# Kernel tuning notes

Hardware: AMD Instinct MI355X
Metric: run time of the kernel (lower is better)

Reference implementation:

```python
import jax, jax.numpy as jnp
import numpy as np

B = 524288
H = 20          # heads
NUM_EX = 13     # embedding rows
EMB = 3         # embedding dim
FEAT_IN, FEAT_OUT = 3, 5
HEAD_IN, HEAD_HID = 8, 10


def setup_inputs() -> dict:
    key = jax.random.key(0)
    ks = jax.random.split(key, 12)
    e = jax.random.randint(ks[0], (B, H), 0, NUM_EX)
    f = jax.random.normal(ks[1], (B, H * FEAT_IN), dtype=jnp.float32)
    # embedding table; row 0 zeroed as in the torch __init__
    emb = jax.random.normal(ks[2], (NUM_EX, EMB), dtype=jnp.float32) * 0.1
    emb = emb.at[0].set(0.0)
    # features Linear(3 -> 5), stored as (in, out) so y = x @ Wf + bf
    Wf = jax.random.normal(ks[3], (FEAT_IN, FEAT_OUT), dtype=jnp.float32) * 0.5
    bf = jax.random.normal(ks[4], (FEAT_OUT,), dtype=jnp.float32) * 0.1
    # 20 parallel head MLPs, batched over the head axis
    W1 = jax.random.normal(ks[5], (H, HEAD_IN, HEAD_HID), dtype=jnp.float32) * 0.3
    b1 = jax.random.normal(ks[6], (H, HEAD_HID), dtype=jnp.float32) * 0.1
    W2 = jax.random.normal(ks[7], (H, HEAD_HID), dtype=jnp.float32) * 0.3
    b2 = jax.random.normal(ks[8], (H,), dtype=jnp.float32) * 0.1
    # output Linear(20 -> 1)
    Wo = jax.random.normal(ks[9], (H, 1), dtype=jnp.float32) * 0.3
    bo = jax.random.normal(ks[10], (1,), dtype=jnp.float32) * 0.1
    return {"e": e, "f": f, "emb": emb, "Wf": Wf, "bf": bf,
            "W1": W1, "b1": b1, "W2": W2, "b2": b2, "Wo": Wo, "bo": bo}


def reference(e, f, emb, Wf, bf, W1, b1, W2, b2, Wo, bo):
    ev = emb[e]                                    # (B, 20, 3) embedding lookup
    fv = f.reshape(-1, H, FEAT_IN) @ Wf + bf       # (B, 20, 5)
    x = jnp.concatenate([ev, fv], axis=2)          # (B, 20, 8)
    # all 20 heads as one batched matmul instead of a Python loop
    h1 = jax.nn.leaky_relu(jnp.einsum('bhi,hio->bho', x, W1) + b1)  # (B, 20, 10)
    h = jax.nn.softplus(jnp.einsum('bho,ho->bh', h1, W2) + b2)      # (B, 20)
    return h @ Wo + bo                             # (B, 1)
```

## Files before the change

kernel.cpp:

```cpp
#include <hip/hip_runtime.h>


#define HH   20
#define NEX  13
#define TST  12
#define WS_M 0
#define WS_T 640

__device__ __forceinline__ float softplus_fast(float x) {
    return fmaxf(x, 0.0f) + __logf(1.0f + __expf(-fabsf(x)));
}

__global__ void airfit_setup(const float* __restrict__ emb,
                             const float* __restrict__ Wf,
                             const float* __restrict__ bf,
                             const float* __restrict__ W1,
                             const float* __restrict__ b1,
                             float* __restrict__ ws)
{
    int t = blockIdx.x * 256 + threadIdx.x;
    if (t < HH * 3 * 10) {
        int h = t / 30, c = (t / 10) % 3, o = t % 10;
        float a = 0.0f;
        for (int q = 0; q < 5; ++q)
            a += Wf[c * 5 + q] * W1[(h * 8 + 3 + q) * 10 + o];
        ws[WS_M + (h * 3 + c) * 10 + o] = a;
    }
    if (t < HH * NEX * 10) {
        int h = t / (NEX * 10), idx = (t / 10) % NEX, o = t % 10;
        float a = b1[h * 10 + o];
        for (int i = 0; i < 3; ++i)
            a += emb[idx * 3 + i] * W1[(h * 8 + i) * 10 + o];
        for (int q = 0; q < 5; ++q)
            a += bf[q] * W1[(h * 8 + 3 + q) * 10 + o];
        ws[WS_T + (h * NEX + idx) * TST + o] = a;
    }
}

__global__ __launch_bounds__(256, 2) void airfit_kernel(
    const int*   __restrict__ e,   const float* __restrict__ f,
    const float* __restrict__ ws,  const float* __restrict__ W2,
    const float* __restrict__ b2,  const float* __restrict__ Wo,
    const float* __restrict__ bo,  float* __restrict__ out, int B)
{
    __shared__ float4       s_f4[15][257];
    __shared__ unsigned int s_ep[256 * 5];
    __shared__ float        s_T[HH * NEX * TST];

    const int tid  = threadIdx.x;
    const int base = blockIdx.x * 256;
    const int nIt  = min(256, B - base);

    for (int t = tid; t < HH * NEX * TST; t += 256)
        s_T[t] = ws[WS_T + t];

    {
        const float4* fg = reinterpret_cast<const float4*>(f) + (size_t)base * 15;
        const int total4 = nIt * 15;
#pragma unroll
        for (int k = 0; k < 15; ++k) {
            int idx = tid + 256 * k;
            if (idx < total4) {
                float4 v = fg[idx];
                int item = idx / 15, c4 = idx - item * 15;
                s_f4[c4][item] = v;
            }
        }
    }

    {
        const int4* eg = reinterpret_cast<const int4*>(e) + (size_t)base * 5;
        const int total4 = nIt * 5;
#pragma unroll
        for (int k = 0; k < 5; ++k) {
            int idx = tid + 256 * k;
            if (idx < total4) {
                int4 iv = eg[idx];
                s_ep[idx] = (unsigned)iv.x | ((unsigned)iv.y << 8) |
                            ((unsigned)iv.z << 16) | ((unsigned)iv.w << 24);
            }
        }
    }

    __syncthreads();

    if (tid >= nIt) return;
    const float* M = ws + WS_M;

    float acc = bo[0];

#pragma unroll
    for (int g = 0; g < 5; ++g) {
        unsigned ep = s_ep[tid * 5 + g];
        float4 fA = s_f4[3 * g + 0][tid];
        float4 fB = s_f4[3 * g + 1][tid];
        float4 fC = s_f4[3 * g + 2][tid];
        float ff[12] = { fA.x, fA.y, fA.z, fA.w,
                         fB.x, fB.y, fB.z, fB.w,
                         fC.x, fC.y, fC.z, fC.w };

#pragma unroll
        for (int t = 0; t < 4; ++t) {
            const int h = 4 * g + t;
            int idx = (ep >> (8 * t)) & 0xff;

            const float* Trow = s_T + (h * NEX + idx) * TST;
            float4 t0 = *reinterpret_cast<const float4*>(Trow);
            float4 t1 = *reinterpret_cast<const float4*>(Trow + 4);
            float2 t2 = *reinterpret_cast<const float2*>(Trow + 8);
            float pre[10] = { t0.x, t0.y, t0.z, t0.w,
                              t1.x, t1.y, t1.z, t1.w, t2.x, t2.y };

            float g0 = ff[3 * t + 0], g1 = ff[3 * t + 1], g2 = ff[3 * t + 2];
            float hacc = b2[h];
#pragma unroll
            for (int o = 0; o < 10; ++o) {
                float a = pre[o];
                a = fmaf(g0, M[(h * 3 + 0) * 10 + o], a);
                a = fmaf(g1, M[(h * 3 + 1) * 10 + o], a);
                a = fmaf(g2, M[(h * 3 + 2) * 10 + o], a);
                a = fmaxf(a, 0.01f * a);
                hacc = fmaf(a, W2[h * 10 + o], hacc);
            }
            acc = fmaf(softplus_fast(hacc), Wo[h], acc);
        }
    }

    out[base + tid] = acc;
}

extern "C" void kernel_launch(void* const* d_in, const int* in_sizes, int n_in,
                              void* d_out, int out_size, void* d_ws, size_t ws_size,
                              hipStream_t stream) {
    const int*   e   = (const int*)  d_in[0];
    const float* f   = (const float*)d_in[1];
    const float* emb = (const float*)d_in[2];
    const float* Wf  = (const float*)d_in[3];
    const float* bf  = (const float*)d_in[4];
    const float* W1  = (const float*)d_in[5];
    const float* b1  = (const float*)d_in[6];
    const float* W2  = (const float*)d_in[7];
    const float* b2  = (const float*)d_in[8];
    const float* Wo  = (const float*)d_in[9];
    const float* bo  = (const float*)d_in[10];
    float* out = (float*)d_out;
    float* ws  = (float*)d_ws;

    int B = in_sizes[0] / HH;

    airfit_setup<<<11, 256, 0, stream>>>(emb, Wf, bf, W1, b1, ws);

    int blocks = (B + 255) / 256;
    airfit_kernel<<<blocks, 256, 0, stream>>>(e, f, ws, W2, b2, Wo, bo, out, B);
}
```

Measured before the change: 274.0 us.

## Store features as fp16 in LDS, pack indices to 4 bits, use 512-thread blocks

Feature values are converted to half precision when staged into shared memory, and embedding indices are packed as 4-bit nibbles into 16-bit words. Both cut LDS use per item so 512-item blocks with a higher occupancy target fit. This rounds the input features to fp16 before the compute, which adds precision error. The removed padding column may add bank conflicts on the transposed writes.

```diff
diff --git a/kernel.cpp b/kernel.cpp
--- a/kernel.cpp
+++ b/kernel.cpp
@@ -6,6 +6,9 @@
 #define TST  12
 #define WS_M 0
 #define WS_T 640
+#define NT   512
+
+typedef __attribute__((ext_vector_type(4))) _Float16 half4;
 
 __device__ __forceinline__ float softplus_fast(float x) {
     return fmaxf(x, 0.0f) + __logf(1.0f + __expf(-fabsf(x)));
@@ -37,21 +40,21 @@
     }
 }
 
-__global__ __launch_bounds__(256, 2) void airfit_kernel(
+__global__ __launch_bounds__(NT, 4) void airfit_kernel(
     const int*   __restrict__ e,   const float* __restrict__ f,
     const float* __restrict__ ws,  const float* __restrict__ W2,
     const float* __restrict__ b2,  const float* __restrict__ Wo,
     const float* __restrict__ bo,  float* __restrict__ out, int B)
 {
-    __shared__ float4       s_f4[15][257];
-    __shared__ unsigned int s_ep[256 * 5];
-    __shared__ float        s_T[HH * NEX * TST];
+    __shared__ half4          s_fh[15][NT];
+    __shared__ unsigned short s_e[NT * 6];
+    __shared__ float          s_T[HH * NEX * TST];
 
     const int tid  = threadIdx.x;
-    const int base = blockIdx.x * 256;
-    const int nIt  = min(256, B - base);
+    const int base = blockIdx.x * NT;
+    const int nIt  = min(NT, B - base);
 
-    for (int t = tid; t < HH * NEX * TST; t += 256)
+    for (int t = tid; t < HH * NEX * TST; t += NT)
         s_T[t] = ws[WS_T + t];
 
     {
@@ -59,11 +62,13 @@
         const int total4 = nIt * 15;
 #pragma unroll
         for (int k = 0; k < 15; ++k) {
-            int idx = tid + 256 * k;
+            int idx = tid + NT * k;
             if (idx < total4) {
                 float4 v = fg[idx];
                 int item = idx / 15, c4 = idx - item * 15;
-                s_f4[c4][item] = v;
+                half4 hv = { (_Float16)v.x, (_Float16)v.y,
+                             (_Float16)v.z, (_Float16)v.w };
+                s_fh[c4][item] = hv;
             }
         }
     }
@@ -73,11 +78,13 @@
         const int total4 = nIt * 5;
 #pragma unroll
         for (int k = 0; k < 5; ++k) {
-            int idx = tid + 256 * k;
+            int idx = tid + NT * k;
             if (idx < total4) {
                 int4 iv = eg[idx];
-                s_ep[idx] = (unsigned)iv.x | ((unsigned)iv.y << 8) |
-                            ((unsigned)iv.z << 16) | ((unsigned)iv.w << 24);
+                int item = idx / 5, g = idx - item * 5;
+                unsigned p = (unsigned)iv.x | ((unsigned)iv.y << 4) |
+                             ((unsigned)iv.z << 8) | ((unsigned)iv.w << 12);
+                s_e[item * 6 + g] = (unsigned short)p;
             }
         }
     }
@@ -87,22 +94,25 @@
     if (tid >= nIt) return;
     const float* M = ws + WS_M;
 
+    const unsigned* e32 = reinterpret_cast<const unsigned*>(s_e);
+    unsigned ew[3] = { e32[tid * 3 + 0], e32[tid * 3 + 1], e32[tid * 3 + 2] };
+
     float acc = bo[0];
 
 #pragma unroll
     for (int g = 0; g < 5; ++g) {
-        unsigned ep = s_ep[tid * 5 + g];
-        float4 fA = s_f4[3 * g + 0][tid];
-        float4 fB = s_f4[3 * g + 1][tid];
-        float4 fC = s_f4[3 * g + 2][tid];
-        float ff[12] = { fA.x, fA.y, fA.z, fA.w,
-                         fB.x, fB.y, fB.z, fB.w,
-                         fC.x, fC.y, fC.z, fC.w };
+        half4 a0 = s_fh[3 * g + 0][tid];
+        half4 a1 = s_fh[3 * g + 1][tid];
+        half4 a2 = s_fh[3 * g + 2][tid];
+        float ff[12] = { (float)a0.x, (float)a0.y, (float)a0.z, (float)a0.w,
+                         (float)a1.x, (float)a1.y, (float)a1.z, (float)a1.w,
+                         (float)a2.x, (float)a2.y, (float)a2.z, (float)a2.w };
+        unsigned gw  = ew[g >> 1] >> ((g & 1) * 16);
 
 #pragma unroll
         for (int t = 0; t < 4; ++t) {
             const int h = 4 * g + t;
-            int idx = (ep >> (8 * t)) & 0xff;
+            int idx = (gw >> (4 * t)) & 0xf;
 
             const float* Trow = s_T + (h * NEX + idx) * TST;
             float4 t0 = *reinterpret_cast<const float4*>(Trow);
@@ -150,6 +160,6 @@
 
     airfit_setup<<<11, 256, 0, stream>>>(emb, Wf, bf, W1, b1, ws);
 
-    int blocks = (B + 255) / 256;
-    airfit_kernel<<<blocks, 256, 0, stream>>>(e, f, ws, W2, b2, Wo, bo, out, B);
+    int blocks = (B + NT - 1) / NT;
+    airfit_kernel<<<blocks, NT, 0, stream>>>(e, f, ws, W2, b2, Wo, bo, out, B);
 }
```

Measured after the change: 251.7 us. 8.1% less time.
